# Kernel tuning notes

Measured on AMD Instinct MI355X. Metric: run time of the kernel, lower is better.

## Reference

```python
import jax, jax.numpy as jnp
import numpy as np

N = 100000   # nodes
E = 200000   # edges
B = 2048     # graphs
D = 256      # embed_dim
L = 5        # gnn layers
NUM_ATOM = 500
NUM_CHI = 500
NUM_BOND_TYPE = 5
NUM_BOND_DIR = 3
BN_EPS = 1e-5


def setup_inputs() -> dict:
    key = jax.random.key(0)
    ks = jax.random.split(key, 20)

    def xavier(k, shape):
        fan_in, fan_out = shape[-2], shape[-1]
        lim = float(np.sqrt(6.0 / (fan_in + fan_out)))
        return jax.random.uniform(k, shape, jnp.float32, -lim, lim)

    inp = {}
    inp["x"] = jax.random.randint(ks[0], (N, 2), 0, NUM_CHI, dtype=jnp.int32)
    inp["edge_index"] = jax.random.randint(ks[1], (2, E), 0, N, dtype=jnp.int32)
    inp["edge_attr"] = jax.random.randint(ks[2], (E, 2), 0, NUM_BOND_DIR, dtype=jnp.int32)
    inp["batch"] = jnp.sort(jax.random.randint(ks[3], (N,), 0, B, dtype=jnp.int32))

    # node embeddings
    inp["x_emb1"] = xavier(ks[4], (NUM_ATOM, D))
    inp["x_emb2"] = xavier(ks[5], (NUM_CHI, D))
    # per-layer edge embeddings (stacked over L layers)
    inp["edge_emb1"] = xavier(ks[6], (L, NUM_BOND_TYPE, D))
    inp["edge_emb2"] = xavier(ks[7], (L, NUM_BOND_DIR, D))
    # per-layer GINE MLP: Linear(D, 2D) -> ReLU -> Linear(2D, D)
    inp["W1"] = xavier(ks[8], (L, D, 2 * D))
    inp["b1"] = jnp.zeros((L, 2 * D), jnp.float32)
    inp["W2"] = xavier(ks[9], (L, 2 * D, D))
    inp["b2"] = jnp.zeros((L, D), jnp.float32)
    # per-layer BatchNorm affine params
    inp["bn_g"] = jnp.ones((L, D), jnp.float32)
    inp["bn_b"] = jnp.zeros((L, D), jnp.float32)
    # output head: Linear(D, D//2) -> Softplus -> Linear(D//2, 2)
    inp["Wo1"] = xavier(ks[10], (D, D // 2))
    inp["bo1"] = jnp.zeros((D // 2,), jnp.float32)
    inp["Wo2"] = xavier(ks[11], (D // 2, 2))
    inp["bo2"] = jnp.zeros((2,), jnp.float32)
    return inp


def reference(x, edge_index, edge_attr, batch,
              x_emb1, x_emb2, edge_emb1, edge_emb2,
              W1, b1, W2, b2, bn_g, bn_b,
              Wo1, bo1, Wo2, bo2):
    n = x.shape[0]
    src, dst = edge_index[0], edge_index[1]
    bt, bd = edge_attr[:, 0], edge_attr[:, 1]

    # initial node features
    h = x_emb1[x[:, 0]] + x_emb2[x[:, 1]]  # [N, D]

    for l in range(L):
        # edge embeddings for real edges
        e = edge_emb1[l][bt] + edge_emb2[l][bd]          # [E, D]
        # self-loop edges carry attr (4, 0)
        self_e = edge_emb1[l][4] + edge_emb2[l][0]       # [D]
        # message = x_j + edge_attr, scatter-add to destination; self-loops add h + self_e
        agg = jax.ops.segment_sum(h[src] + e, dst, num_segments=n) + h + self_e
        # GINE update MLP
        z = jax.nn.relu(agg @ W1[l] + b1[l]) @ W2[l] + b2[l]
        # BatchNorm1d (training-mode batch statistics, biased variance)
        mu = z.mean(axis=0)
        var = z.var(axis=0)
        z = (z - mu) / jnp.sqrt(var + BN_EPS) * bn_g[l] + bn_b[l]
        h = jax.nn.relu(z)  # dropout=0 -> identity

    # global mean pool over graphs
    cnt = jax.ops.segment_sum(jnp.ones((n,), h.dtype), batch, num_segments=B)
    pooled = jax.ops.segment_sum(h, batch, num_segments=B) / jnp.maximum(cnt, 1.0)[:, None]

    # output head (y.size(0) != 2 so proj_head is skipped)
    out = jax.nn.softplus(pooled @ Wo1 + bo1) @ Wo2 + bo2  # [B, 2]
    return out
```

## Files before the change

kernel.cpp:

```cpp
#include <hip/hip_runtime.h>

#define NNODES 100000
#define NEDGES 200000
#define NB     2048
#define DIM    256
#define NLAYERS 5
#define NSB    98

typedef __bf16 bf16x8 __attribute__((ext_vector_type(8)));
typedef float  f32x4  __attribute__((ext_vector_type(4)));

__device__ __forceinline__ float bf2f(unsigned short u) {
    union { unsigned u; float f; } v; v.u = ((unsigned)u) << 16; return v.f;
}
__device__ __forceinline__ unsigned short f2bf(float f) {
    union { float f; unsigned u; } v; v.f = f;
    unsigned r = v.u + 0x7fff + ((v.u >> 16) & 1);
    return (unsigned short)(r >> 16);
}
__device__ __forceinline__ float4 loadZ4(const unsigned short* z, size_t row, int ch) {
    ushort4 u = *(const ushort4*)&z[row * DIM + ch];
    float4 r; r.x = bf2f(u.x); r.y = bf2f(u.y); r.z = bf2f(u.z); r.w = bf2f(u.w); return r;
}

__global__ void zero_i32(int* __restrict__ p, int n) {
    int i = blockIdx.x * 256 + threadIdx.x;
    if (i < n) p[i] = 0;
}

__global__ void transpose_w(const float* __restrict__ W,
                            unsigned short* __restrict__ Wt, int K, int Nw) {
    int l = blockIdx.y;
    int t = blockIdx.x * 256 + threadIdx.x;
    int total = K * Nw;
    if (t >= total) return;
    int k = t / Nw, n = t % Nw;
    Wt[(size_t)l * total + (size_t)n * K + k] = f2bf(W[(size_t)l * total + t]);
}

__global__ void build_etab(const float* __restrict__ ee1, const float* __restrict__ ee2,
                           float* __restrict__ etab) {
    int l = blockIdx.y, c = blockIdx.x, d = threadIdx.x;
    etab[((size_t)l * 15 + c) * DIM + d] =
        ee1[((size_t)l * 5 + c / 3) * DIM + d] + ee2[((size_t)l * 3 + c % 3) * DIM + d];
}

__global__ void csr_hist(const int* __restrict__ ei, int* __restrict__ deg) {
    int j = blockIdx.x * 256 + threadIdx.x;
    if (j < NEDGES) atomicAdd(&deg[ei[NEDGES + j]], 1);
}
__global__ __launch_bounds__(1024) void scan_blk(const int* __restrict__ deg,
                                                 int* __restrict__ rowptr,
                                                 int* __restrict__ bsum) {
    __shared__ int s[1024];
    int b = blockIdx.x, t = threadIdx.x, i = b * 1024 + t;
    s[t] = (i < NNODES) ? deg[i] : 0;
    __syncthreads();
    #pragma unroll
    for (int off = 1; off < 1024; off <<= 1) {
        int u = (t >= off) ? s[t - off] : 0;
        __syncthreads();
        s[t] += u;
        __syncthreads();
    }
    if (i < NNODES) rowptr[i + 1] = s[t];
    if (t == 1023) bsum[b] = s[1023];
}
__global__ void scan_partials(int* __restrict__ bsum) {
    if (threadIdx.x == 0) {
        int acc = 0;
        for (int k = 0; k < NSB; ++k) { acc += bsum[k]; bsum[k] = acc; }
    }
}
__global__ void scan_add(int* __restrict__ rowptr, const int* __restrict__ bsum) {
    int b = blockIdx.x, t = threadIdx.x, i = b * 1024 + t;
    if (b > 0 && i < NNODES) rowptr[i + 1] += bsum[b - 1];
    if (b == 0 && t == 0) rowptr[0] = 0;
}
__global__ void csr_fill(const int* __restrict__ ei, const int* __restrict__ ea,
                         const int* __restrict__ rowptr, int* __restrict__ deg,
                         int* __restrict__ esrc, int* __restrict__ eattr) {
    int j = blockIdx.x * 256 + threadIdx.x;
    if (j >= NEDGES) return;
    int d = ei[NEDGES + j];
    int pos = atomicSub(&deg[d], 1) - 1;
    int slot = rowptr[d] + pos;
    esrc[slot] = ei[j];
    eattr[slot] = ea[2 * j] * 3 + ea[2 * j + 1];
}

__global__ void seg_starts(const int* __restrict__ batch, int* __restrict__ start) {
    int g = blockIdx.x * 256 + threadIdx.x;
    if (g > NB) return;
    int lo = 0, hi = NNODES;
    while (lo < hi) { int mid = (lo + hi) >> 1; if (batch[mid] < g) lo = mid + 1; else hi = mid; }
    start[g] = lo;
}

template <int MODE>
__global__ __launch_bounds__(256) void gather_k(const unsigned short* __restrict__ z,
                                                const int* __restrict__ x,
                                                const float* __restrict__ xe1,
                                                const float* __restrict__ xe2,
                                                const float* __restrict__ statsP,
                                                const float* __restrict__ g_,
                                                const float* __restrict__ b_,
                                                float* __restrict__ statsZ,
                                                const float* __restrict__ etab_l,
                                                const int* __restrict__ rowptr,
                                                const int* __restrict__ esrc,
                                                const int* __restrict__ eattr,
                                                unsigned short* __restrict__ agg) {
    if (blockIdx.x == 0) { statsZ[threadIdx.x] = 0.f; statsZ[256 + threadIdx.x] = 0.f; }
    int i = blockIdx.x * 4 + (threadIdx.x >> 6);
    int lane = threadIdx.x & 63, ch = lane * 4;

    float4 a4, c4;
    if (MODE == 1) {
        float4 s4 = *(const float4*)&statsP[ch];
        float4 q4 = *(const float4*)&statsP[256 + ch];
        float4 g4 = *(const float4*)&g_[ch];
        float4 b4 = *(const float4*)&b_[ch];
        const float invN = 1.0f / (float)NNODES;
        float mux = s4.x * invN, muy = s4.y * invN, muz = s4.z * invN, muw = s4.w * invN;
        a4.x = g4.x * rsqrtf(q4.x * invN - mux * mux + 1e-5f);
        a4.y = g4.y * rsqrtf(q4.y * invN - muy * muy + 1e-5f);
        a4.z = g4.z * rsqrtf(q4.z * invN - muz * muz + 1e-5f);
        a4.w = g4.w * rsqrtf(q4.w * invN - muw * muw + 1e-5f);
        c4.x = b4.x - mux * a4.x; c4.y = b4.y - muy * a4.y;
        c4.z = b4.z - muz * a4.z; c4.w = b4.w - muw * a4.w;
    }

    auto hrow = [&](int row) -> float4 {
        if (MODE == 0) {
            int i0 = x[2 * row], i1 = x[2 * row + 1];
            float4 u = *(const float4*)&xe1[(size_t)i0 * DIM + ch];
            float4 v = *(const float4*)&xe2[(size_t)i1 * DIM + ch];
            return make_float4(u.x + v.x, u.y + v.y, u.z + v.z, u.w + v.w);
        } else {
            float4 h = loadZ4(z, (size_t)row, ch);
            h.x = fmaxf(h.x * a4.x + c4.x, 0.f); h.y = fmaxf(h.y * a4.y + c4.y, 0.f);
            h.z = fmaxf(h.z * a4.z + c4.z, 0.f); h.w = fmaxf(h.w * a4.w + c4.w, 0.f);
            return h;
        }
    };

    float4 se = *(const float4*)&etab_l[12 * DIM + ch];
    float4 hv = hrow(i);
    float4 acc = make_float4(hv.x + se.x, hv.y + se.y, hv.z + se.z, hv.w + se.w);

    int r0 = rowptr[i], r1 = rowptr[i + 1];
    int e = r0;
    for (; e + 2 <= r1; e += 2) {
        int s0 = esrc[e], c0 = eattr[e];
        int s1 = esrc[e + 1], c1 = eattr[e + 1];
        float4 h0 = hrow(s0);
        float4 h1 = hrow(s1);
        float4 e0 = *(const float4*)&etab_l[c0 * DIM + ch];
        float4 e1 = *(const float4*)&etab_l[c1 * DIM + ch];
        acc.x += h0.x + e0.x + h1.x + e1.x; acc.y += h0.y + e0.y + h1.y + e1.y;
        acc.z += h0.z + e0.z + h1.z + e1.z; acc.w += h0.w + e0.w + h1.w + e1.w;
    }
    if (e < r1) {
        int s0 = esrc[e], c0 = eattr[e];
        float4 h0 = hrow(s0);
        float4 e0 = *(const float4*)&etab_l[c0 * DIM + ch];
        acc.x += h0.x + e0.x; acc.y += h0.y + e0.y;
        acc.z += h0.z + e0.z; acc.w += h0.w + e0.w;
    }
    ushort4 o; o.x = f2bf(acc.x); o.y = f2bf(acc.y); o.z = f2bf(acc.z); o.w = f2bf(acc.w);
    *(ushort4*)&agg[(size_t)i * DIM + ch] = o;
}

__global__ __launch_bounds__(512, 4) void mlp64(const unsigned short* __restrict__ agg,
                                                const unsigned short* __restrict__ Wt1,
                                                const float* __restrict__ b1,
                                                const unsigned short* __restrict__ Wt2,
                                                const float* __restrict__ b2,
                                                unsigned short* __restrict__ z,
                                                float* __restrict__ stats) {
    __shared__ unsigned short Ts[64 * 520];

    const int rowBase = blockIdx.x * 64;
    const int tid = threadIdx.x;
    const int lane = tid & 63, w = tid >> 6;
    const int lrow = lane & 15, lq = lane >> 4;

    {
        f32x4 acc[4][4]{};
        #pragma unroll
        for (int kk = 0; kk < DIM / 32; ++kk) {
            const int kc = kk * 32 + lq * 8;
            bf16x8 a[4], b[4];
            #pragma unroll
            for (int mi = 0; mi < 4; ++mi) {
                int row = rowBase + mi * 16 + lrow; if (row >= NNODES) row = NNODES - 1;
                a[mi] = *(const bf16x8*)&agg[(size_t)row * DIM + kc];
            }
            #pragma unroll
            for (int ni = 0; ni < 4; ++ni)
                b[ni] = *(const bf16x8*)&Wt1[(size_t)(w * 64 + ni * 16 + lrow) * DIM + kc];
            #pragma unroll
            for (int mi = 0; mi < 4; ++mi)
                #pragma unroll
                for (int ni = 0; ni < 4; ++ni)
                    acc[mi][ni] = __builtin_amdgcn_mfma_f32_16x16x32_bf16(a[mi], b[ni], acc[mi][ni], 0, 0, 0);
        }
        #pragma unroll
        for (int ni = 0; ni < 4; ++ni) {
            int col = w * 64 + ni * 16 + lrow;
            float bv = b1[col];
            #pragma unroll
            for (int mi = 0; mi < 4; ++mi)
                #pragma unroll
                for (int r = 0; r < 4; ++r)
                    Ts[(mi * 16 + lq * 4 + r) * 520 + col] = f2bf(fmaxf(acc[mi][ni][r] + bv, 0.f));
        }
    }
    __syncthreads();

    {
        f32x4 acc[4][2]{};
        #pragma unroll
        for (int kk = 0; kk < 2 * DIM / 32; ++kk) {
            const int kc = kk * 32 + lq * 8;
            bf16x8 a[4], b[2];
            #pragma unroll
            for (int mi = 0; mi < 4; ++mi)
                a[mi] = *(const bf16x8*)&Ts[(mi * 16 + lrow) * 520 + kc];
            #pragma unroll
            for (int ni = 0; ni < 2; ++ni)
                b[ni] = *(const bf16x8*)&Wt2[(size_t)(w * 32 + ni * 16 + lrow) * (2 * DIM) + kc];
            #pragma unroll
            for (int mi = 0; mi < 4; ++mi)
                #pragma unroll
                for (int ni = 0; ni < 2; ++ni)
                    acc[mi][ni] = __builtin_amdgcn_mfma_f32_16x16x32_bf16(a[mi], b[ni], acc[mi][ni], 0, 0, 0);
        }
        #pragma unroll
        for (int ni = 0; ni < 2; ++ni) {
            int col = w * 32 + ni * 16 + lrow;
            float bv = b2[col];
            float s = 0.f, q = 0.f;
            #pragma unroll
            for (int mi = 0; mi < 4; ++mi)
                #pragma unroll
                for (int r = 0; r < 4; ++r) {
                    int row = rowBase + mi * 16 + lq * 4 + r;
                    if (row < NNODES) {
                        float v = acc[mi][ni][r] + bv;
                        z[(size_t)row * DIM + col] = f2bf(v);
                        s += v; q += v * v;
                    }
                }
            s += __shfl_xor(s, 16); s += __shfl_xor(s, 32);
            q += __shfl_xor(q, 16); q += __shfl_xor(q, 32);
            if (lq == 0) {
                atomicAdd(&stats[col], s);
                atomicAdd(&stats[DIM + col], q);
            }
        }
    }
}

__global__ __launch_bounds__(256) void pool_seg(const unsigned short* __restrict__ z,
                                                const float* __restrict__ statsP,
                                                const float* __restrict__ g_,
                                                const float* __restrict__ b_,
                                                const int* __restrict__ start,
                                                float* __restrict__ pooled) {
    int g = blockIdx.x, ch = threadIdx.x;
    float mu = statsP[ch] / (float)NNODES;
    float var = statsP[256 + ch] / (float)NNODES - mu * mu;
    float a = g_[ch] * rsqrtf(var + 1e-5f);
    float c = b_[ch] - mu * a;
    int r0 = start[g], r1 = start[g + 1];
    float s = 0.f;
    for (int i = r0; i < r1; ++i)
        s += fmaxf(bf2f(z[(size_t)i * DIM + ch]) * a + c, 0.f);
    pooled[(size_t)g * DIM + ch] = s / fmaxf((float)(r1 - r0), 1.f);
}

__global__ __launch_bounds__(128) void head_mlp(const float* __restrict__ pooled,
                                                const float* __restrict__ Wo1,
                                                const float* __restrict__ bo1,
                                                const float* __restrict__ Wo2,
                                                const float* __restrict__ bo2,
                                                float* __restrict__ out) {
    __shared__ float p[DIM];
    __shared__ float r0[128], r1[128];
    int g = blockIdx.x, j = threadIdx.x;
    for (int k = j; k < DIM; k += 128) p[k] = pooled[(size_t)g * DIM + k];
    __syncthreads();
    float acc = bo1[j];
    for (int k = 0; k < DIM; ++k) acc += p[k] * Wo1[k * 128 + j];
    float sp = (acc > 20.f) ? acc : log1pf(expf(acc));
    r0[j] = sp * Wo2[j * 2 + 0];
    r1[j] = sp * Wo2[j * 2 + 1];
    __syncthreads();
    for (int s = 64; s > 0; s >>= 1) {
        if (j < s) { r0[j] += r0[j + s]; r1[j] += r1[j + s]; }
        __syncthreads();
    }
    if (j == 0) {
        out[g * 2 + 0] = r0[0] + bo2[0];
        out[g * 2 + 1] = r1[0] + bo2[1];
    }
}

extern "C" void kernel_launch(void* const* d_in, const int* in_sizes, int n_in,
                              void* d_out, int out_size, void* d_ws, size_t ws_size,
                              hipStream_t stream) {
    (void)in_sizes; (void)n_in; (void)out_size;
    const int* x     = (const int*)d_in[0];
    const int* ei    = (const int*)d_in[1];
    const int* ea    = (const int*)d_in[2];
    const int* batch = (const int*)d_in[3];
    const float* xe1 = (const float*)d_in[4];
    const float* xe2 = (const float*)d_in[5];
    const float* ee1 = (const float*)d_in[6];
    const float* ee2 = (const float*)d_in[7];
    const float* W1  = (const float*)d_in[8];
    const float* b1  = (const float*)d_in[9];
    const float* W2  = (const float*)d_in[10];
    const float* b2  = (const float*)d_in[11];
    const float* bng = (const float*)d_in[12];
    const float* bnb = (const float*)d_in[13];
    const float* Wo1 = (const float*)d_in[14];
    const float* bo1 = (const float*)d_in[15];
    const float* Wo2 = (const float*)d_in[16];
    const float* bo2 = (const float*)d_in[17];
    float* out = (float*)d_out;

    if (ws_size < 112000000ull) return;

    char* ws = (char*)d_ws;
    size_t off = 0;
    auto alloc = [&](size_t bytes) { void* p = ws + off; off += (bytes + 255) & ~255ull; return p; };
    unsigned short* z   = (unsigned short*)alloc((size_t)NNODES * DIM * 2);
    unsigned short* agg = (unsigned short*)alloc((size_t)NNODES * DIM * 2);
    unsigned short* Wt1 = (unsigned short*)alloc((size_t)NLAYERS * DIM * 2 * DIM * 2);
    unsigned short* Wt2 = (unsigned short*)alloc((size_t)NLAYERS * DIM * 2 * DIM * 2);
    float* etab         = (float*)alloc((size_t)NLAYERS * 15 * DIM * 4);
    float* stats        = (float*)alloc(2 * 512 * 4);
    float* pooled       = (float*)alloc((size_t)NB * DIM * 4);
    int* gstart         = (int*)alloc((size_t)(NB + 1) * 4);
    int* rowptr         = (int*)alloc((size_t)(NNODES + 1) * 4);
    int* deg            = (int*)alloc((size_t)NNODES * 4);
    int* esrc           = (int*)alloc((size_t)NEDGES * 4);
    int* eattr          = (int*)alloc((size_t)NEDGES * 4);
    int* bsum           = (int*)alloc((size_t)NSB * 4);

    const int WTOT = DIM * 2 * DIM;

    transpose_w<<<dim3((WTOT + 255) / 256, NLAYERS), 256, 0, stream>>>(W1, Wt1, DIM, 2 * DIM);
    transpose_w<<<dim3((WTOT + 255) / 256, NLAYERS), 256, 0, stream>>>(W2, Wt2, 2 * DIM, DIM);
    build_etab<<<dim3(15, NLAYERS), DIM, 0, stream>>>(ee1, ee2, etab);

    zero_i32<<<(NNODES + 255) / 256, 256, 0, stream>>>(deg, NNODES);
    csr_hist<<<(NEDGES + 255) / 256, 256, 0, stream>>>(ei, deg);
    scan_blk<<<NSB, 1024, 0, stream>>>(deg, rowptr, bsum);
    scan_partials<<<1, 64, 0, stream>>>(bsum);
    scan_add<<<NSB, 1024, 0, stream>>>(rowptr, bsum);
    csr_fill<<<(NEDGES + 255) / 256, 256, 0, stream>>>(ei, ea, rowptr, deg, esrc, eattr);
    seg_starts<<<(NB + 1 + 255) / 256, 256, 0, stream>>>(batch, gstart);

    for (int l = 0; l < NLAYERS; ++l) {
        float* statsP = stats + ((l + 1) & 1) * 512;
        float* statsC = stats + (l & 1) * 512;
        if (l == 0)
            gather_k<0><<<NNODES / 4, 256, 0, stream>>>(z, x, xe1, xe2, statsP, bng, bnb, statsC,
                                                        etab, rowptr, esrc, eattr, agg);
        else
            gather_k<1><<<NNODES / 4, 256, 0, stream>>>(z, x, xe1, xe2, statsP,
                                                        bng + (size_t)(l - 1) * DIM, bnb + (size_t)(l - 1) * DIM,
                                                        statsC, etab + (size_t)l * 15 * DIM,
                                                        rowptr, esrc, eattr, agg);
        mlp64<<<(NNODES + 63) / 64, 512, 0, stream>>>(agg, Wt1 + (size_t)l * WTOT, b1 + l * 2 * DIM,
                                                      Wt2 + (size_t)l * WTOT, b2 + l * DIM, z, statsC);
    }

    pool_seg<<<NB, DIM, 0, stream>>>(z, stats + ((NLAYERS - 1) & 1) * 512,
                                     bng + (size_t)(NLAYERS - 1) * DIM, bnb + (size_t)(NLAYERS - 1) * DIM,
                                     gstart, pooled);
    head_mlp<<<NB, 128, 0, stream>>>(pooled, Wo1, bo1, Wo2, bo2, out);
}
```

Measured before the change: 1.308 ms.

## Stage agg tile in LDS and chunk hidden dim to shrink LDS and registers

The MLP kernel now copies the 64-row agg tile into shared memory once, then processes the 512-wide hidden layer in four 128-column chunks. Each chunk's ReLU output goes into a smaller LDS buffer and is consumed immediately by the second GEMM, accumulating into persistent accumulators. This replaces per-wave global reloads of agg and cuts LDS and accumulator register use, which lets launch_bounds ask for 6 blocks per CU. In exchange it adds extra barriers per chunk and reloads the second weight matrix in slices.

```diff
diff --git a/kernel.cpp b/kernel.cpp
--- a/kernel.cpp
+++ b/kernel.cpp
@@ -172,93 +172,96 @@
     *(ushort4*)&agg[(size_t)i * DIM + ch] = o;
 }
 
-__global__ __launch_bounds__(512, 4) void mlp64(const unsigned short* __restrict__ agg,
+__global__ __launch_bounds__(512, 6) void mlp64(const unsigned short* __restrict__ agg,
                                                 const unsigned short* __restrict__ Wt1,
                                                 const float* __restrict__ b1,
                                                 const unsigned short* __restrict__ Wt2,
                                                 const float* __restrict__ b2,
                                                 unsigned short* __restrict__ z,
                                                 float* __restrict__ stats) {
-    __shared__ unsigned short Ts[64 * 520];
+    __shared__ unsigned short As[64 * 264];
+    __shared__ unsigned short Ts[64 * 136];
 
     const int rowBase = blockIdx.x * 64;
     const int tid = threadIdx.x;
     const int lane = tid & 63, w = tid >> 6;
     const int lrow = lane & 15, lq = lane >> 4;
 
-    {
-        f32x4 acc[4][4]{};
+    #pragma unroll
+    for (int c = tid; c < 64 * 32; c += 512) {
+        int r = c >> 5, cc = c & 31;
+        int row = rowBase + r; if (row >= NNODES) row = NNODES - 1;
+        *(uint4*)&As[r * 264 + cc * 8] = *(const uint4*)&agg[(size_t)row * DIM + cc * 8];
+    }
+    f32x4 acc2[4][2]{};
+    __syncthreads();
+
+    #pragma unroll
+    for (int q = 0; q < 4; ++q) {
+        f32x4 acc1[4]{};
+        const unsigned short* w1p = &Wt1[(size_t)(q * 128 + w * 16 + lrow) * DIM];
         #pragma unroll
-        for (int kk = 0; kk < DIM / 32; ++kk) {
+        for (int kk = 0; kk < 8; ++kk) {
             const int kc = kk * 32 + lq * 8;
-            bf16x8 a[4], b[4];
-            #pragma unroll
-            for (int mi = 0; mi < 4; ++mi) {
-                int row = rowBase + mi * 16 + lrow; if (row >= NNODES) row = NNODES - 1;
-                a[mi] = *(const bf16x8*)&agg[(size_t)row * DIM + kc];
-            }
-            #pragma unroll
-            for (int ni = 0; ni < 4; ++ni)
-                b[ni] = *(const bf16x8*)&Wt1[(size_t)(w * 64 + ni * 16 + lrow) * DIM + kc];
-            #pragma unroll
-            for (int mi = 0; mi < 4; ++mi)
-                #pragma unroll
-                for (int ni = 0; ni < 4; ++ni)
-                    acc[mi][ni] = __builtin_amdgcn_mfma_f32_16x16x32_bf16(a[mi], b[ni], acc[mi][ni], 0, 0, 0);
-        }
-        #pragma unroll
-        for (int ni = 0; ni < 4; ++ni) {
-            int col = w * 64 + ni * 16 + lrow;
-            float bv = b1[col];
+            bf16x8 b = *(const bf16x8*)&w1p[kc];
+            bf16x8 a[4];
+            #pragma unroll
+            for (int mi = 0; mi < 4; ++mi)
+                a[mi] = *(const bf16x8*)&As[(mi * 16 + lrow) * 264 + kc];
+            #pragma unroll
+            for (int mi = 0; mi < 4; ++mi)
+                acc1[mi] = __builtin_amdgcn_mfma_f32_16x16x32_bf16(a[mi], b, acc1[mi], 0, 0, 0);
+        }
+        if (q > 0) __syncthreads();
+        {
+            int col = w * 16 + lrow;
+            float bv = b1[q * 128 + col];
             #pragma unroll
             for (int mi = 0; mi < 4; ++mi)
                 #pragma unroll
                 for (int r = 0; r < 4; ++r)
-                    Ts[(mi * 16 + lq * 4 + r) * 520 + col] = f2bf(fmaxf(acc[mi][ni][r] + bv, 0.f));
-        }
-    }
-    __syncthreads();
-
-    {
-        f32x4 acc[4][2]{};
+                    Ts[(mi * 16 + lq * 4 + r) * 136 + col] = f2bf(fmaxf(acc1[mi][r] + bv, 0.f));
+        }
+        __syncthreads();
         #pragma unroll
-        for (int kk = 0; kk < 2 * DIM / 32; ++kk) {
+        for (int kk = 0; kk < 4; ++kk) {
             const int kc = kk * 32 + lq * 8;
             bf16x8 a[4], b[2];
             #pragma unroll
             for (int mi = 0; mi < 4; ++mi)
-                a[mi] = *(const bf16x8*)&Ts[(mi * 16 + lrow) * 520 + kc];
+                a[mi] = *(const bf16x8*)&Ts[(mi * 16 + lrow) * 136 + kc];
             #pragma unroll
             for (int ni = 0; ni < 2; ++ni)
-                b[ni] = *(const bf16x8*)&Wt2[(size_t)(w * 32 + ni * 16 + lrow) * (2 * DIM) + kc];
+                b[ni] = *(const bf16x8*)&Wt2[(size_t)(w * 32 + ni * 16 + lrow) * (2 * DIM) + q * 128 + kc];
             #pragma unroll
             for (int mi = 0; mi < 4; ++mi)
                 #pragma unroll
                 for (int ni = 0; ni < 2; ++ni)
-                    acc[mi][ni] = __builtin_amdgcn_mfma_f32_16x16x32_bf16(a[mi], b[ni], acc[mi][ni], 0, 0, 0);
-        }
+                    acc2[mi][ni] = __builtin_amdgcn_mfma_f32_16x16x32_bf16(a[mi], b[ni], acc2[mi][ni], 0, 0, 0);
+        }
+    }
+
+    #pragma unroll
+    for (int ni = 0; ni < 2; ++ni) {
+        int col = w * 32 + ni * 16 + lrow;
+        float bv = b2[col];
+        float s = 0.f, q = 0.f;
         #pragma unroll
-        for (int ni = 0; ni < 2; ++ni) {
-            int col = w * 32 + ni * 16 + lrow;
-            float bv = b2[col];
-            float s = 0.f, q = 0.f;
-            #pragma unroll
-            for (int mi = 0; mi < 4; ++mi)
-                #pragma unroll
-                for (int r = 0; r < 4; ++r) {
-                    int row = rowBase + mi * 16 + lq * 4 + r;
-                    if (row < NNODES) {
-                        float v = acc[mi][ni][r] + bv;
-                        z[(size_t)row * DIM + col] = f2bf(v);
-                        s += v; q += v * v;
-                    }
+        for (int mi = 0; mi < 4; ++mi)
+            #pragma unroll
+            for (int r = 0; r < 4; ++r) {
+                int row = rowBase + mi * 16 + lq * 4 + r;
+                if (row < NNODES) {
+                    float v = acc2[mi][ni][r] + bv;
+                    z[(size_t)row * DIM + col] = f2bf(v);
+                    s += v; q += v * v;
                 }
-            s += __shfl_xor(s, 16); s += __shfl_xor(s, 32);
-            q += __shfl_xor(q, 16); q += __shfl_xor(q, 32);
-            if (lq == 0) {
-                atomicAdd(&stats[col], s);
-                atomicAdd(&stats[DIM + col], q);
             }
+        s += __shfl_xor(s, 16); s += __shfl_xor(s, 32);
+        q += __shfl_xor(q, 16); q += __shfl_xor(q, 32);
+        if (lq == 0) {
+            atomicAdd(&stats[col], s);
+            atomicAdd(&stats[DIM + col], q);
         }
     }
 }
```

After: 1.101 ms. 15.8% less time.
